# Optimization experiments

Measured on AMD Instinct MI355X. Metric: run time of the kernel, lower is better.

Reference implementation:

```python
import jax, jax.numpy as jnp
import numpy as np

USER_NUM = 100000
POI_NUM = 120
EMB = 64
HID1, HID2 = 256, 128
HEADS, ATT_H = 6, 8
SEQ = 5
CI_VOCAB = 50000
N_EDGES_U = 1600000


def _gcn_conv(x, edge_index, W, b, n):
    # PyG GCNConv: add self loops, symmetric D^-1/2 (A+I) D^-1/2 normalization
    x = x @ W
    loops = jnp.arange(n)
    src = jnp.concatenate([edge_index[0], loops])
    dst = jnp.concatenate([edge_index[1], loops])
    deg = jax.ops.segment_sum(jnp.ones_like(dst, x.dtype), dst, num_segments=n)
    dinv = jnp.where(deg > 0, jax.lax.rsqrt(deg), 0.0)
    norm = dinv[src] * dinv[dst]
    out = jax.ops.segment_sum(x[src] * norm[:, None], dst, num_segments=n)
    return out + b


def setup_inputs() -> dict:
    key = jax.random.key(0)
    ks = jax.random.split(key, 30)
    f = lambda k, shape, fan_in: (jax.random.normal(k, shape, jnp.float32) / np.sqrt(fan_in)).astype(jnp.float32)
    inp = {}
    inp['edge_user'] = jnp.stack([
        jax.random.randint(ks[0], (USER_NUM, SEQ), 0, USER_NUM),
        jax.random.randint(ks[1], (USER_NUM, SEQ), 0, CI_VOCAB)])
    inp['edge_poi'] = jax.random.randint(ks[2], (2, 4000), 0, POI_NUM)
    inp['u_v_edge'] = jax.random.randint(ks[3], (2, N_EDGES_U), 0, USER_NUM)
    inp['v_u_edge'] = jax.random.randint(ks[4], (2, 4000), 0, POI_NUM)
    inp['user_table'] = f(ks[5], (USER_NUM, EMB), EMB)
    inp['ci_table'] = f(ks[6], (CI_VOCAB, EMB), EMB)
    inp['ci_table2'] = f(ks[7], (CI_VOCAB, EMB), EMB)
    inp['gcn1_w'] = f(ks[8], (EMB, EMB), EMB)
    inp['gcn1_b'] = jnp.zeros((EMB,), jnp.float32)
    inp['gcn2_w'] = f(ks[9], (EMB, EMB), EMB)
    inp['gcn2_b'] = jnp.zeros((EMB,), jnp.float32)
    inp['at_w'] = f(ks[10], (HEADS, EMB, ATT_H), EMB)
    inp['at_b'] = jnp.zeros((HEADS, ATT_H), jnp.float32)
    inp['d2_w'] = f(ks[11], (1 + HEADS * ATT_H, 1), 1 + HEADS * ATT_H)  # Linear(49,1)
    inp['d2_b'] = jnp.zeros((1,), jnp.float32)
    inp['d1u_w'] = f(ks[12], (EMB, HID1), EMB)
    inp['d1u_b'] = jnp.zeros((HID1,), jnp.float32)
    inp['d2u_w'] = f(ks[13], (HID1, HID2), HID1)
    inp['d2u_b'] = jnp.zeros((HID2,), jnp.float32)
    inp['d3u_w'] = f(ks[14], (HID2, POI_NUM), HID2)
    inp['d3u_b'] = jnp.zeros((POI_NUM,), jnp.float32)
    inp['d1_w'] = f(ks[15], (EMB, POI_NUM), EMB)  # dense1_: Linear(n_emb, 120)
    inp['d1_b'] = jnp.zeros((POI_NUM,), jnp.float32)
    return inp


def reference(edge_user, edge_poi, u_v_edge, v_u_edge, user_table, ci_table, ci_table2,
              gcn1_w, gcn1_b, gcn2_w, gcn2_b, at_w, at_b, d2_w, d2_b,
              d1u_w, d1u_b, d2u_w, d2u_b, d3u_w, d3u_b, d1_w, d1_b):
    # user GCN stack (dropout treated as identity / eval mode)
    ue = _gcn_conv(user_table, u_v_edge, gcn1_w, gcn1_b, USER_NUM)
    ue = jax.nn.relu(ue)
    ue = _gcn_conv(ue, u_v_edge, gcn2_w, gcn2_b, USER_NUM)  # (U, EMB)

    ci_ids = edge_user[1]            # (U, SEQ) check-in ids
    ci = ci_table[ci_ids]            # (U, SEQ, EMB)
    ci2 = ci_table2[ci_ids]          # (U, SEQ, EMB)

    # batched multi-head tiny attention: softmax over the SEQ axis per user
    w = jnp.einsum('usd,hdk->uhsk', ci, at_w) + at_b[None, :, None, :]
    beta = jax.nn.softmax(jnp.tanh(w), axis=2)                       # (U, H, SEQ, ATT_H)
    beta = jnp.transpose(beta, (0, 2, 1, 3)).reshape(ci.shape[0], SEQ, HEADS * ATT_H)
    att = jnp.transpose(beta, (0, 2, 1))                              # (U, 48, SEQ)
    use_trans = att @ ci                                              # (U, 48, EMB)

    uef = jnp.concatenate([ue[:, None, :], use_trans], axis=1)       # (U, 49, EMB)
    uef = jnp.transpose(uef, (0, 2, 1)) @ d2_w + d2_b                # (U, EMB, 1)
    uef = uef[..., 0]                                                # (U, EMB)

    h = jax.nn.relu(uef @ d1u_w + d1u_b)
    h = jax.nn.relu(h @ d2u_w + d2u_b)
    score1 = h @ d3u_w + d3u_b                                       # (U, POI_NUM)

    score2 = jnp.sum(ci2 @ d1_w + d1_b, axis=1)                      # (U, POI_NUM)
    return score1 + score2
```

## Files before the change

### kernel.cpp

```cpp
#include <hip/hip_runtime.h>

#define U_NUM 100000
#define NE    1600000
#define SEQL  5

#define OFF_DEG      0UL
#define OFF_ROWSTART 800000UL
#define OFF_DINV     1200016UL
#define OFF_BSUM     1600016UL
#define OFF_CSR      1600528UL
#define OFF_XS       8000528UL
#define OFF_B        20800528UL
#define OFF_CI2B     46400528UL
#define OFF_CIB      52800528UL

#define NB    196
#define BSH   9
#define BCAP  12240
#define OFF_BINS  OFF_XS
#define OFF_GCUR  (OFF_BINS + (size_t)NB * BCAP * 8)

typedef __attribute__((ext_vector_type(8))) short bf16x8;
typedef __attribute__((ext_vector_type(4))) float f32x4;
typedef __attribute__((ext_vector_type(4))) unsigned u32x4;

__device__ __forceinline__ float rd_lane(float v, int l) {
    return __int_as_float(__builtin_amdgcn_readlane(__float_as_int(v), l));
}

__device__ __forceinline__ short f2bf(float f) {
    unsigned u = __float_as_uint(f);
    unsigned r = (u + 0x7fffu + ((u >> 16) & 1u)) >> 16;
    return (short)r;
}

__device__ __forceinline__ unsigned pk2(float a, float b) {
    return ((unsigned)(unsigned short)f2bf(a)) | (((unsigned)(unsigned short)f2bf(b)) << 16);
}

__device__ __forceinline__ float bflo(unsigned p) { return __uint_as_float(p << 16); }
__device__ __forceinline__ float bfhi(unsigned p) { return __uint_as_float(p & 0xffff0000u); }

__device__ __forceinline__ int swzo(int row, int bytecol, int rowstride) {
    return row * rowstride + (bytecol ^ ((row & 7) << 4));
}

__global__ __launch_bounds__(256) void k_count(const int* __restrict__ edge, int* __restrict__ deg) {
    int e = blockIdx.x * 256 + threadIdx.x;
    atomicAdd(&deg[edge[NE + e]], 1);
}

__global__ __launch_bounds__(256) void k_dinv(const int* __restrict__ deg, float* __restrict__ dinv) {
    int i = blockIdx.x * 256 + threadIdx.x;
    if (i < U_NUM) dinv[i] = rsqrtf((float)(deg[i] + 1));
}

__global__ __launch_bounds__(256) void k_cvt2(const float* __restrict__ src, unsigned* __restrict__ dst) {
    int i = blockIdx.x * 256 + threadIdx.x;
    float2 v = *(const float2*)(src + (size_t)i * 2);
    dst[i] = pk2(v.x, v.y);
}

__global__ __launch_bounds__(1024) void k_scanA(const int* __restrict__ deg, int* __restrict__ bsum) {
    __shared__ int sm[1024];
    int i = blockIdx.x * 1024 + threadIdx.x;
    sm[threadIdx.x] = (i < U_NUM) ? deg[i] : 0;
    __syncthreads();
    for (int off = 512; off > 0; off >>= 1) {
        if (threadIdx.x < off) sm[threadIdx.x] += sm[threadIdx.x + off];
        __syncthreads();
    }
    if (threadIdx.x == 0) bsum[blockIdx.x] = sm[0];
}

__global__ void k_scanB(int* bsum, int nb) {
    if (threadIdx.x == 0) {
        int acc = 0;
        for (int b = 0; b < nb; ++b) { int v = bsum[b]; bsum[b] = acc; acc += v; }
    }
}

__global__ __launch_bounds__(1024) void k_scanC(const int* __restrict__ deg, const int* __restrict__ bsum,
                                                int* __restrict__ row_start) {
    __shared__ int sm[1024];
    int t = threadIdx.x;
    int i = blockIdx.x * 1024 + t;
    int v = (i < U_NUM) ? deg[i] : 0;
    sm[t] = v;
    __syncthreads();
    for (int off = 1; off < 1024; off <<= 1) {
        int x = (t >= off) ? sm[t - off] : 0;
        __syncthreads();
        sm[t] += x;
        __syncthreads();
    }
    int incl = sm[t];
    int base = bsum[blockIdx.x];
    if (i < U_NUM) row_start[i] = base + incl - v;
    if (i == U_NUM - 1) row_start[U_NUM] = base + incl;
}

__global__ __launch_bounds__(256) void k_binA(const int* __restrict__ edge,
                                              unsigned* __restrict__ gcur,
                                              uint2* __restrict__ bins) {
    __shared__ int hist[256];
    __shared__ int startx[256];
    __shared__ int cur[256];
    __shared__ int gbase[256];
    __shared__ uint2 stage[4096];
    int t = threadIdx.x;
    int base = blockIdx.x * 4096;
    hist[t] = 0; cur[t] = 0;
    __syncthreads();
    int src[16], dst[16];
#pragma unroll
    for (int j = 0; j < 16; ++j) {
        int e = base + j * 256 + t;
        src[j] = 0; dst[j] = -1;
        if (e < NE) {
            src[j] = edge[e];
            dst[j] = edge[NE + e];
            atomicAdd(&hist[dst[j] >> BSH], 1);
        }
    }
    __syncthreads();
    startx[t] = hist[t];
    __syncthreads();
    for (int off = 1; off < 256; off <<= 1) {
        int v = (t >= off) ? startx[t - off] : 0;
        __syncthreads();
        startx[t] += v;
        __syncthreads();
    }
    {
        int ex = startx[t] - hist[t];
        __syncthreads();
        startx[t] = ex;
    }
    if (t < NB) gbase[t] = (int)atomicAdd(&gcur[t], (unsigned)hist[t]);
    __syncthreads();
#pragma unroll
    for (int j = 0; j < 16; ++j) {
        if (dst[j] >= 0) {
            int b = dst[j] >> BSH;
            int p = startx[b] + atomicAdd(&cur[b], 1);
            stage[p] = make_uint2((unsigned)src[j], (unsigned)dst[j]);
        }
    }
    __syncthreads();
    int cnt = NE - base; if (cnt > 4096) cnt = 4096;
    for (int p = t; p < cnt; p += 256) {
        uint2 v = stage[p];
        int b = (int)(v.y >> BSH);
        bins[(size_t)b * BCAP + gbase[b] + (p - startx[b])] = v;
    }
}

__global__ __launch_bounds__(256) void k_fillB(const uint2* __restrict__ bins,
                                               const unsigned* __restrict__ gcur,
                                               const int* __restrict__ row_start,
                                               int* __restrict__ csr) {
    __shared__ int cur[512];
    int b = blockIdx.x, t = threadIdx.x;
    cur[t] = 0; cur[t + 256] = 0;
    __syncthreads();
    int cnt = (int)gcur[b];
    int d0 = b << BSH;
    for (int i = t; i < cnt; i += 256) {
        uint2 e = bins[(size_t)b * BCAP + i];
        int d = (int)e.y;
        int pos = row_start[d] + atomicAdd(&cur[d - d0], 1);
        csr[pos] = (int)e.x;
    }
}

__global__ __launch_bounds__(256) void k_gemm64_mfma(
        const float* __restrict__ x, const float* __restrict__ w,
        const float* __restrict__ dinv, unsigned* __restrict__ outb, int relu_in) {
    __shared__ __align__(16) short Xa[64 * 64];
    __shared__ float dv[64];
    int t = threadIdx.x;
    int lane = t & 63, wid = t >> 6;
    int l15 = lane & 15, lg = lane >> 4;
    bf16x8 wf[2];
#pragma unroll
    for (int ks = 0; ks < 2; ++ks) {
        int col = wid * 16 + l15;
        int kb = ks * 32 + lg * 8;
        bf16x8 f;
#pragma unroll
        for (int j = 0; j < 8; ++j) f[j] = f2bf(w[(kb + j) * 64 + col]);
        wf[ks] = f;
    }
    int u0 = blockIdx.x * 64;
    {
        int ur = t >> 2, d0 = (t & 3) * 16;
        int u = u0 + ur;
        float xv[16];
        if (u < U_NUM) {
            const float4* up = (const float4*)(x + (size_t)u * 64 + d0);
#pragma unroll
            for (int q = 0; q < 4; ++q) {
                float4 v = up[q];
                xv[q * 4 + 0] = v.x; xv[q * 4 + 1] = v.y; xv[q * 4 + 2] = v.z; xv[q * 4 + 3] = v.w;
            }
        } else {
#pragma unroll
            for (int q = 0; q < 16; ++q) xv[q] = 0.f;
        }
        if (relu_in) {
#pragma unroll
            for (int q = 0; q < 16; ++q) xv[q] = fmaxf(xv[q], 0.f);
        }
        bf16x8 p0, p1;
#pragma unroll
        for (int j = 0; j < 8; ++j) { p0[j] = f2bf(xv[j]); p1[j] = f2bf(xv[8 + j]); }
        *(bf16x8*)((char*)Xa + swzo(ur, d0 * 2, 128)) = p0;
        *(bf16x8*)((char*)Xa + swzo(ur, d0 * 2 + 16, 128)) = p1;
        if (t < 64) {
            int uu = u0 + t;
            dv[t] = dinv[(uu < U_NUM) ? uu : (U_NUM - 1)];
        }
    }
    __syncthreads();
#pragma unroll
    for (int mt = 0; mt < 4; ++mt) {
        bf16x8 a0 = *(bf16x8*)((char*)Xa + swzo(mt * 16 + l15, lg * 16, 128));
        bf16x8 a1 = *(bf16x8*)((char*)Xa + swzo(mt * 16 + l15, 64 + lg * 16, 128));
        f32x4 c = {0.f, 0.f, 0.f, 0.f};
        c = __builtin_amdgcn_mfma_f32_16x16x32_bf16(a0, wf[0], c, 0, 0, 0);
        c = __builtin_amdgcn_mfma_f32_16x16x32_bf16(a1, wf[1], c, 0, 0, 0);
        int col = wid * 16 + l15;
#pragma unroll
        for (int r = 0; r < 4; ++r) {
            int row = mt * 16 + lg * 4 + r;
            float v = c[r] * dv[row];
            float other = __shfl_xor(v, 1);
            int u = u0 + row;
            if (!(l15 & 1) && u < U_NUM)
                outb[(size_t)u * 32 + (col >> 1)] = pk2(v, other);
        }
    }
}

__global__ __launch_bounds__(256) void k_gather2(const unsigned* __restrict__ xs, const float* __restrict__ dinv,
                                                 const int* __restrict__ row_start, const int* __restrict__ csr,
                                                 const float* __restrict__ bias, float* __restrict__ outb) {
    int i = blockIdx.x * 4 + (threadIdx.x >> 6);
    int lane = threadIdx.x & 63, half = lane >> 5, sl = lane & 31;
    int s0 = row_start[i], s1 = row_start[i + 1];
    float di = dinv[i];
    float accx = 0.f, accy = 0.f;
    if (!half) {
        unsigned pk = xs[(size_t)i * 32 + sl];
        accx = bflo(pk); accy = bfhi(pk);
    }
    int e = s0 + half;
    for (; e + 14 < s1; e += 16) {
        int id0 = csr[e], id1 = csr[e + 2], id2 = csr[e + 4], id3 = csr[e + 6];
        int id4 = csr[e + 8], id5 = csr[e + 10], id6 = csr[e + 12], id7 = csr[e + 14];
        unsigned p0 = xs[(size_t)id0 * 32 + sl];
        unsigned p1 = xs[(size_t)id1 * 32 + sl];
        unsigned p2 = xs[(size_t)id2 * 32 + sl];
        unsigned p3 = xs[(size_t)id3 * 32 + sl];
        unsigned p4 = xs[(size_t)id4 * 32 + sl];
        unsigned p5 = xs[(size_t)id5 * 32 + sl];
        unsigned p6 = xs[(size_t)id6 * 32 + sl];
        unsigned p7 = xs[(size_t)id7 * 32 + sl];
        accx += ((bflo(p0) + bflo(p1)) + (bflo(p2) + bflo(p3))) +
                ((bflo(p4) + bflo(p5)) + (bflo(p6) + bflo(p7)));
        accy += ((bfhi(p0) + bfhi(p1)) + (bfhi(p2) + bfhi(p3))) +
                ((bfhi(p4) + bfhi(p5)) + (bfhi(p6) + bfhi(p7)));
    }
    for (; e < s1; e += 2) {
        unsigned pa = xs[(size_t)csr[e] * 32 + sl];
        accx += bflo(pa);
        accy += bfhi(pa);
    }
    accx += __shfl_xor(accx, 32);
    accy += __shfl_xor(accy, 32);
    if (!half) {
        float2 bb = *(const float2*)(bias + sl * 2);
        float2 o;
        o.x = fmaf(accx, di, bb.x);
        o.y = fmaf(accy, di, bb.y);
        *(float2*)(outb + (size_t)i * 64 + sl * 2) = o;
    }
}

#define AUB 32

__global__ __launch_bounds__(256) void k_attn_mfma(
        const int* __restrict__ edge_user, const unsigned* __restrict__ cib,
        const unsigned* __restrict__ ci2b,
        const float* __restrict__ at_w, const float* __restrict__ at_b,
        const float* __restrict__ d2_w, const float* __restrict__ d2_b,
        const float* ue, unsigned* uefc) {
    __shared__ __align__(16) short CI[256 * 64];
    int t = threadIdx.x;
    int lane = t & 63, wid = t >> 6;
    int l15 = lane & 15, lg = lane >> 4;
    int half = lane >> 5, sl = lane & 31;

    bf16x8 bw[3][2];
#pragma unroll
    for (int nt = 0; nt < 3; ++nt) {
        int j48 = nt * 16 + l15;
        int h = j48 >> 3, kk = j48 & 7;
#pragma unroll
        for (int ks = 0; ks < 2; ++ks) {
            int kb = ks * 32 + lg * 8;
            bf16x8 f;
#pragma unroll
            for (int j = 0; j < 8; ++j) f[j] = f2bf(at_w[h * 512 + (kb + j) * 8 + kk]);
            bw[nt][ks] = f;
        }
    }
    float atbv[3], dcoef[3];
#pragma unroll
    for (int nt = 0; nt < 3; ++nt) {
        atbv[nt] = at_b[nt * 16 + l15];
        dcoef[nt] = d2_w[1 + nt * 16 + l15];
    }
    float d2w0 = d2_w[0], d2b0 = d2_b[0];

    int u0 = blockIdx.x * AUB;
    float accx[8], accy[8];
#pragma unroll
    for (int j = 0; j < 8; ++j) { accx[j] = 0.f; accy[j] = 0.f; }
#pragma unroll
    for (int j = 0; j < 8; ++j) {
#pragma unroll
        for (int q = 0; q < 4; ++q) {
            int s = q * 2 + half;
            int row = wid * 64 + j * 8 + s;
            unsigned pk = 0;
            if (s < 5) {
                int id = edge_user[U_NUM * SEQL + (u0 + wid * 8 + j) * SEQL + s];
                pk = cib[(size_t)id * 32 + sl];
                unsigned pc = ci2b[(size_t)id * 32 + sl];
                accx[j] += bflo(pc);
                accy[j] += bfhi(pc);
            }
            *(unsigned*)((char*)CI + swzo(row, sl * 4, 128)) = pk;
        }
    }
    __syncthreads();

    float evenm = (lg & 1) ? 0.f : 1.f;
    for (int mt = 0; mt < 4; ++mt) {
        int tbase = (wid * 4 + mt) * 16;
        bf16x8 a0 = *(bf16x8*)((char*)CI + swzo(tbase + l15, lg * 16, 128));
        bf16x8 a1 = *(bf16x8*)((char*)CI + swzo(tbase + l15, 64 + lg * 16, 128));
        float g0 = 0.f, g1 = 0.f, g2 = 0.f, g3 = 0.f;
#pragma unroll
        for (int nt = 0; nt < 3; ++nt) {
            f32x4 c = {0.f, 0.f, 0.f, 0.f};
            c = __builtin_amdgcn_mfma_f32_16x16x32_bf16(a0, bw[nt][0], c, 0, 0, 0);
            c = __builtin_amdgcn_mfma_f32_16x16x32_bf16(a1, bw[nt][1], c, 0, 0, 0);
            float w0 = c[0] + atbv[nt], w1 = c[1] + atbv[nt],
                  w2 = c[2] + atbv[nt], w3 = c[3] + atbv[nt];
            float e0 = __expf(1.f - __fdividef(2.f, __expf(2.f * w0) + 1.f));
            float e1 = __expf(1.f - __fdividef(2.f, __expf(2.f * w1) + 1.f));
            float e2 = __expf(1.f - __fdividef(2.f, __expf(2.f * w2) + 1.f));
            float e3 = __expf(1.f - __fdividef(2.f, __expf(2.f * w3) + 1.f));
            float partial = e0 + evenm * (e1 + e2 + e3);
            float esum = partial + __shfl_xor(partial, 16);
            float sc = __fdividef(dcoef[nt], esum);
            g0 = fmaf(e0, sc, g0);
            g1 = fmaf(e1, sc, g1);
            g2 = fmaf(e2, sc, g2);
            g3 = fmaf(e3, sc, g3);
        }
#pragma unroll
        for (int d = 1; d < 16; d <<= 1) {
            g0 += __shfl_xor(g0, d);
            g1 += __shfl_xor(g1, d);
            g2 += __shfl_xor(g2, d);
            g3 += __shfl_xor(g3, d);
        }
        float gA0 = rd_lane(g0, 0), gA1 = rd_lane(g1, 0), gA2 = rd_lane(g2, 0),
              gA3 = rd_lane(g3, 0), gA4 = rd_lane(g0, 16);
        float gB0 = rd_lane(g0, 32), gB1 = rd_lane(g1, 32), gB2 = rd_lane(g2, 32),
              gB3 = rd_lane(g3, 32), gB4 = rd_lane(g0, 48);
        float gs0 = half ? gB0 : gA0;
        float gs1 = half ? gB1 : gA1;
        float gs2 = half ? gB2 : gA2;
        float gs3 = half ? gB3 : gA3;
        float gs4 = half ? gB4 : gA4;
        int urow = tbase + half * 8;
        int u = u0 + (tbase >> 3) + half;
        float2 uev = *(const float2*)(ue + (size_t)u * 64 + sl * 2);
        float rx = fmaf(d2w0, uev.x, d2b0);
        float ry = fmaf(d2w0, uev.y, d2b0);
        unsigned c0 = *(unsigned*)((char*)CI + swzo(urow + 0, sl * 4, 128));
        unsigned c1 = *(unsigned*)((char*)CI + swzo(urow + 1, sl * 4, 128));
        unsigned c2 = *(unsigned*)((char*)CI + swzo(urow + 2, sl * 4, 128));
        unsigned c3 = *(unsigned*)((char*)CI + swzo(urow + 3, sl * 4, 128));
        unsigned c4 = *(unsigned*)((char*)CI + swzo(urow + 4, sl * 4, 128));
        rx = fmaf(gs0, bflo(c0), rx); ry = fmaf(gs0, bfhi(c0), ry);
        rx = fmaf(gs1, bflo(c1), rx); ry = fmaf(gs1, bfhi(c1), ry);
        rx = fmaf(gs2, bflo(c2), rx); ry = fmaf(gs2, bfhi(c2), ry);
        rx = fmaf(gs3, bflo(c3), rx); ry = fmaf(gs3, bfhi(c3), ry);
        rx = fmaf(gs4, bflo(c4), rx); ry = fmaf(gs4, bfhi(c4), ry);
        uefc[(size_t)u * 64 + sl] = pk2(rx, ry);
    }
#pragma unroll
    for (int j = 0; j < 8; ++j) {
        float ax = accx[j] + __shfl_xor(accx[j], 32);
        float ay = accy[j] + __shfl_xor(accy[j], 32);
        if (!half) {
            int u = u0 + wid * 8 + j;
            uefc[(size_t)u * 64 + 32 + sl] = pk2(ax, ay);
        }
    }
}

#define N_TILES 1563

__global__ __launch_bounds__(512, 4) void k_mlp_mfma(
        const unsigned* __restrict__ uefc,
        const float* __restrict__ w1, const float* __restrict__ b1,
        const float* __restrict__ w2, const float* __restrict__ b2,
        const float* __restrict__ w3, const float* __restrict__ b3,
        const float* __restrict__ dw, const float* __restrict__ db,
        float* __restrict__ out) {
    __shared__ __align__(16) short Xa[64 * 64];
    __shared__ __align__(16) short Ca[64 * 64];
    __shared__ __align__(16) short h1a[64 * 256];
    __shared__ __align__(16) short h2c[64 * 128];
    int t = threadIdx.x;
    int lane = t & 63, w = t >> 6;
    int l15 = lane & 15, lg = lane >> 4;

    bf16x8 wf1[4];
#pragma unroll
    for (int nt = 0; nt < 2; ++nt)
#pragma unroll
        for (int ks = 0; ks < 2; ++ks) {
            int col = w * 32 + nt * 16 + l15;
            int kb = ks * 32 + lg * 8;
            bf16x8 f;
#pragma unroll
            for (int j = 0; j < 8; ++j) f[j] = f2bf(w1[(kb + j) * 256 + col]);
            wf1[nt * 2 + ks] = f;
        }
    bf16x8 wf2[8];
#pragma unroll
    for (int ks = 0; ks < 8; ++ks) {
        int col = w * 16 + l15;
        int kb = ks * 32 + lg * 8;
        bf16x8 f;
#pragma unroll
        for (int j = 0; j < 8; ++j) f[j] = f2bf(w2[(kb + j) * 128 + col]);
        wf2[ks] = f;
    }
    bf16x8 wf3[6];
#pragma unroll
    for (int ks = 0; ks < 6; ++ks) {
        int col = w * 16 + l15;
        int kb = ks * 32 + lg * 8;
        bf16x8 f;
#pragma unroll
        for (int j = 0; j < 8; ++j) {
            int k = kb + j;
            float v = 0.f;
            if (col < 120) v = (k < 128) ? w3[k * 120 + col] : dw[(k - 128) * 120 + col];
            f[j] = f2bf(v);
        }
        wf3[ks] = f;
    }
    float bias1[2], bias2, bias3;
#pragma unroll
    for (int nt = 0; nt < 2; ++nt) bias1[nt] = b1[w * 32 + nt * 16 + l15];
    {
        int col = w * 16 + l15;
        bias2 = b2[col];
        bias3 = (col < 120) ? (b3[col] + 5.f * db[col]) : 0.f;
    }

    int ur = t >> 3, q = t & 7;
    for (int tile = blockIdx.x; tile < N_TILES; tile += gridDim.x) {
        int u0 = tile * 64;
        {
            size_t u = (size_t)u0 + ur;
            u32x4 A0 = {0, 0, 0, 0}, A1 = A0;
            if (u < U_NUM) {
                const u32x4* up = (const u32x4*)(uefc + u * 64 + q * 8);
                A0 = __builtin_nontemporal_load(up);
                A1 = __builtin_nontemporal_load(up + 1);
            }
            char* base = (q < 4) ? ((char*)Xa) : ((char*)Ca);
            int bc = (q & 3) * 32;
            *(u32x4*)(base + swzo(ur, bc, 128)) = A0;
            *(u32x4*)(base + swzo(ur, bc + 16, 128)) = A1;
        }
        __syncthreads();
#pragma unroll
        for (int mt = 0; mt < 4; ++mt) {
            bf16x8 a0 = *(bf16x8*)((char*)Xa + swzo(mt * 16 + l15, lg * 16, 128));
            bf16x8 a1 = *(bf16x8*)((char*)Xa + swzo(mt * 16 + l15, 64 + lg * 16, 128));
#pragma unroll
            for (int nt = 0; nt < 2; ++nt) {
                f32x4 c = {0.f, 0.f, 0.f, 0.f};
                c = __builtin_amdgcn_mfma_f32_16x16x32_bf16(a0, wf1[nt * 2 + 0], c, 0, 0, 0);
                c = __builtin_amdgcn_mfma_f32_16x16x32_bf16(a1, wf1[nt * 2 + 1], c, 0, 0, 0);
                int col = w * 32 + nt * 16 + l15;
                float bb = bias1[nt];
#pragma unroll
                for (int r = 0; r < 4; ++r) {
                    int row = mt * 16 + lg * 4 + r;
                    *(short*)((char*)h1a + swzo(row, col * 2, 512)) = f2bf(fmaxf(c[r] + bb, 0.f));
                }
            }
        }
        __syncthreads();
#pragma unroll
        for (int mt = 0; mt < 4; ++mt) {
            bf16x8 af[8];
#pragma unroll
            for (int ks = 0; ks < 8; ++ks)
                af[ks] = *(bf16x8*)((char*)h1a + swzo(mt * 16 + l15, ks * 64 + lg * 16, 512));
            f32x4 c = {0.f, 0.f, 0.f, 0.f};
#pragma unroll
            for (int ks = 0; ks < 8; ++ks)
                c = __builtin_amdgcn_mfma_f32_16x16x32_bf16(af[ks], wf2[ks], c, 0, 0, 0);
            int col = w * 16 + l15;
#pragma unroll
            for (int r = 0; r < 4; ++r) {
                int row = mt * 16 + lg * 4 + r;
                *(short*)((char*)h2c + swzo(row, col * 2, 256)) = f2bf(fmaxf(c[r] + bias2, 0.f));
            }
        }
        __syncthreads();
        float* Obuf = (float*)h1a;
#pragma unroll
        for (int mt = 0; mt < 4; ++mt) {
            bf16x8 af[6];
#pragma unroll
            for (int ks = 0; ks < 4; ++ks)
                af[ks] = *(bf16x8*)((char*)h2c + swzo(mt * 16 + l15, ks * 64 + lg * 16, 256));
#pragma unroll
            for (int ks = 4; ks < 6; ++ks)
                af[ks] = *(bf16x8*)((char*)Ca + swzo(mt * 16 + l15, (ks - 4) * 64 + lg * 16, 128));
            f32x4 c = {0.f, 0.f, 0.f, 0.f};
#pragma unroll
            for (int ks = 0; ks < 6; ++ks)
                c = __builtin_amdgcn_mfma_f32_16x16x32_bf16(af[ks], wf3[ks], c, 0, 0, 0);
            int col = w * 16 + l15;
            if (col < 120) {
#pragma unroll
                for (int r = 0; r < 4; ++r)
                    Obuf[(mt * 16 + lg * 4 + r) * 124 + col] = c[r] + bias3;
            }
        }
        __syncthreads();
        {
            int nrow = (U_NUM - u0 < 64) ? (U_NUM - u0) : 64;
            int nfl4 = nrow * 30;
            for (int i = t; i < nfl4; i += 512) {
                int row = i / 30, ch = i - row * 30;
                f32x4 v = *(const f32x4*)(Obuf + row * 124 + ch * 4);
                __builtin_nontemporal_store(v, (f32x4*)(out + (size_t)(u0 + row) * 120 + ch * 4));
            }
        }
        __syncthreads();
    }
}

extern "C" void kernel_launch(void* const* d_in, const int* in_sizes, int n_in,
                              void* d_out, int out_size, void* d_ws, size_t ws_size,
                              hipStream_t stream) {
    const int* edge_user   = (const int*)d_in[0];
    const int* u_v_edge    = (const int*)d_in[2];
    const float* user_table = (const float*)d_in[4];
    const float* ci_table   = (const float*)d_in[5];
    const float* ci_table2  = (const float*)d_in[6];
    const float* gcn1_w = (const float*)d_in[7];
    const float* gcn1_b = (const float*)d_in[8];
    const float* gcn2_w = (const float*)d_in[9];
    const float* gcn2_b = (const float*)d_in[10];
    const float* at_w = (const float*)d_in[11];
    const float* at_b = (const float*)d_in[12];
    const float* d2_w = (const float*)d_in[13];
    const float* d2_b = (const float*)d_in[14];
    const float* d1u_w = (const float*)d_in[15];
    const float* d1u_b = (const float*)d_in[16];
    const float* d2u_w = (const float*)d_in[17];
    const float* d2u_b = (const float*)d_in[18];
    const float* d3u_w = (const float*)d_in[19];
    const float* d3u_b = (const float*)d_in[20];
    const float* d1_w = (const float*)d_in[21];
    const float* d1_b = (const float*)d_in[22];
    float* out = (float*)d_out;
    char* ws = (char*)d_ws;

    int* deg       = (int*)(ws + OFF_DEG);
    int* row_start = (int*)(ws + OFF_ROWSTART);
    float* dinv    = (float*)(ws + OFF_DINV);
    int* bsum      = (int*)(ws + OFF_BSUM);
    int* csr       = (int*)(ws + OFF_CSR);
    unsigned* XS   = (unsigned*)(ws + OFF_XS);
    float* B       = (float*)(ws + OFF_B);
    unsigned* CI2B = (unsigned*)(ws + OFF_CI2B);
    unsigned* CIB  = (unsigned*)(ws + OFF_CIB);
    uint2* bins    = (uint2*)(ws + OFF_BINS);
    unsigned* gcur = (unsigned*)(ws + OFF_GCUR);

    (void)hipMemsetAsync(ws, 0, 400000, stream);
    (void)hipMemsetAsync(ws + OFF_GCUR, 0, NB * 4, stream);
    k_count<<<6250, 256, 0, stream>>>(u_v_edge, deg);
    k_cvt2<<<6250, 256, 0, stream>>>(ci_table, CIB);
    k_cvt2<<<6250, 256, 0, stream>>>(ci_table2, CI2B);
    k_dinv<<<391, 256, 0, stream>>>(deg, dinv);
    k_scanA<<<98, 1024, 0, stream>>>(deg, bsum);
    k_scanB<<<1, 64, 0, stream>>>(bsum, 98);
    k_scanC<<<98, 1024, 0, stream>>>(deg, bsum, row_start);
    k_binA<<<391, 256, 0, stream>>>(u_v_edge, gcur, bins);
    k_fillB<<<NB, 256, 0, stream>>>(bins, gcur, row_start, csr);

    k_gemm64_mfma<<<1563, 256, 0, stream>>>(user_table, gcn1_w, dinv, XS, 0);
    k_gather2<<<25000, 256, 0, stream>>>(XS, dinv, row_start, csr, gcn1_b, B);
    k_gemm64_mfma<<<1563, 256, 0, stream>>>(B, gcn2_w, dinv, XS, 1);
    k_gather2<<<25000, 256, 0, stream>>>(XS, dinv, row_start, csr, gcn2_b, B);

    k_attn_mfma<<<3125, 256, 0, stream>>>(edge_user, CIB, CI2B, at_w, at_b, d2_w, d2_b,
                                          B, (unsigned*)B);
    k_mlp_mfma<<<512, 512, 0, stream>>>((const unsigned*)B,
                                        d1u_w, d1u_b, d2u_w, d2u_b, d3u_w, d3u_b, d1_w, d1_b, out);
}
```

Measured before the change: 468.9 us.

## Restructure MLP kernel to 32-row tiles with 16 waves and split-K reductions

The final MLP kernel now processes 32-user tiles with 1024-thread blocks. Layers 2 and 3 are split along K across two wave groups, and the partial sums are combined through a shared float buffer. Each wave holds fewer weight fragments, which cuts register pressure and raises parallelism per tile. The cost is extra barriers and LDS round-trips per tile. The tail check is dropped, which is safe only because 100000 divides evenly by 32.

```diff
diff --git a/kernel.cpp b/kernel.cpp
--- a/kernel.cpp
+++ b/kernel.cpp
@@ -22,7 +22,7 @@
 
 typedef __attribute__((ext_vector_type(8))) short bf16x8;
 typedef __attribute__((ext_vector_type(4))) float f32x4;
-typedef __attribute__((ext_vector_type(4))) unsigned u32x4;
+typedef __attribute__((ext_vector_type(2))) unsigned u32x2;
 
 __device__ __forceinline__ float rd_lane(float v, int l) {
     return __int_as_float(__builtin_amdgcn_readlane(__float_as_int(v), l));
@@ -416,153 +416,150 @@
     }
 }
 
-#define N_TILES 1563
-
-__global__ __launch_bounds__(512, 4) void k_mlp_mfma(
+#define N_TILES2 3125
+
+__global__ __launch_bounds__(1024, 2) void k_mlp_mfma(
         const unsigned* __restrict__ uefc,
         const float* __restrict__ w1, const float* __restrict__ b1,
         const float* __restrict__ w2, const float* __restrict__ b2,
         const float* __restrict__ w3, const float* __restrict__ b3,
         const float* __restrict__ dw, const float* __restrict__ db,
         float* __restrict__ out) {
-    __shared__ __align__(16) short Xa[64 * 64];
-    __shared__ __align__(16) short Ca[64 * 64];
-    __shared__ __align__(16) short h1a[64 * 256];
-    __shared__ __align__(16) short h2c[64 * 128];
+    __shared__ __align__(16) short Xa[32 * 64];
+    __shared__ __align__(16) short Ca[32 * 64];
+    __shared__ __align__(16) short h1a[32 * 256];
+    __shared__ __align__(16) short h2c[32 * 128];
+    __shared__ __align__(16) float Pf[32 * 128];
     int t = threadIdx.x;
     int lane = t & 63, w = t >> 6;
     int l15 = lane & 15, lg = lane >> 4;
-
-    bf16x8 wf1[4];
-#pragma unroll
-    for (int nt = 0; nt < 2; ++nt)
-#pragma unroll
-        for (int ks = 0; ks < 2; ++ks) {
-            int col = w * 32 + nt * 16 + l15;
-            int kb = ks * 32 + lg * 8;
-            bf16x8 f;
-#pragma unroll
-            for (int j = 0; j < 8; ++j) f[j] = f2bf(w1[(kb + j) * 256 + col]);
-            wf1[nt * 2 + ks] = f;
-        }
-    bf16x8 wf2[8];
-#pragma unroll
-    for (int ks = 0; ks < 8; ++ks) {
-        int col = w * 16 + l15;
+    int nt = w & 7, kh = w >> 3;
+    int col1 = w * 16 + l15;
+    int col2 = nt * 16 + l15;
+
+    bf16x8 wf1[2];
+#pragma unroll
+    for (int ks = 0; ks < 2; ++ks) {
         int kb = ks * 32 + lg * 8;
         bf16x8 f;
 #pragma unroll
-        for (int j = 0; j < 8; ++j) f[j] = f2bf(w2[(kb + j) * 128 + col]);
+        for (int j = 0; j < 8; ++j) f[j] = f2bf(w1[(kb + j) * 256 + col1]);
+        wf1[ks] = f;
+    }
+    bf16x8 wf2[4];
+#pragma unroll
+    for (int ks = 0; ks < 4; ++ks) {
+        int kb = kh * 128 + ks * 32 + lg * 8;
+        bf16x8 f;
+#pragma unroll
+        for (int j = 0; j < 8; ++j) f[j] = f2bf(w2[(kb + j) * 128 + col2]);
         wf2[ks] = f;
     }
-    bf16x8 wf3[6];
-#pragma unroll
-    for (int ks = 0; ks < 6; ++ks) {
-        int col = w * 16 + l15;
-        int kb = ks * 32 + lg * 8;
+    bf16x8 wf3[3];
+#pragma unroll
+    for (int ks = 0; ks < 3; ++ks) {
         bf16x8 f;
 #pragma unroll
         for (int j = 0; j < 8; ++j) {
-            int k = kb + j;
+            int k = kh * 96 + ks * 32 + lg * 8 + j;
             float v = 0.f;
-            if (col < 120) v = (k < 128) ? w3[k * 120 + col] : dw[(k - 128) * 120 + col];
+            if (col2 < 120) v = (k < 128) ? w3[k * 120 + col2] : dw[(k - 128) * 120 + col2];
             f[j] = f2bf(v);
         }
         wf3[ks] = f;
     }
-    float bias1[2], bias2, bias3;
-#pragma unroll
-    for (int nt = 0; nt < 2; ++nt) bias1[nt] = b1[w * 32 + nt * 16 + l15];
-    {
-        int col = w * 16 + l15;
-        bias2 = b2[col];
-        bias3 = (col < 120) ? (b3[col] + 5.f * db[col]) : 0.f;
-    }
-
-    int ur = t >> 3, q = t & 7;
-    for (int tile = blockIdx.x; tile < N_TILES; tile += gridDim.x) {
-        int u0 = tile * 64;
+    float bias1 = b1[col1];
+    float bias2 = b2[col2];
+    float bias3 = (col2 < 120) ? (b3[col2] + 5.f * db[col2]) : 0.f;
+
+    int ur = t >> 5, q = t & 31;
+    for (int tile = blockIdx.x; tile < N_TILES2; tile += gridDim.x) {
+        int u0 = tile * 32;
         {
-            size_t u = (size_t)u0 + ur;
-            u32x4 A0 = {0, 0, 0, 0}, A1 = A0;
-            if (u < U_NUM) {
-                const u32x4* up = (const u32x4*)(uefc + u * 64 + q * 8);
-                A0 = __builtin_nontemporal_load(up);
-                A1 = __builtin_nontemporal_load(up + 1);
-            }
-            char* base = (q < 4) ? ((char*)Xa) : ((char*)Ca);
-            int bc = (q & 3) * 32;
-            *(u32x4*)(base + swzo(ur, bc, 128)) = A0;
-            *(u32x4*)(base + swzo(ur, bc + 16, 128)) = A1;
-        }
-        __syncthreads();
-#pragma unroll
-        for (int mt = 0; mt < 4; ++mt) {
+            const u32x2* up = (const u32x2*)(uefc + (size_t)(u0 + ur) * 64 + q * 2);
+            u32x2 A = __builtin_nontemporal_load(up);
+            char* base = (q < 16) ? ((char*)Xa) : ((char*)Ca);
+            *(u32x2*)(base + swzo(ur, (q & 15) * 8, 128)) = A;
+        }
+        __syncthreads();
+#pragma unroll
+        for (int mt = 0; mt < 2; ++mt) {
             bf16x8 a0 = *(bf16x8*)((char*)Xa + swzo(mt * 16 + l15, lg * 16, 128));
             bf16x8 a1 = *(bf16x8*)((char*)Xa + swzo(mt * 16 + l15, 64 + lg * 16, 128));
-#pragma unroll
-            for (int nt = 0; nt < 2; ++nt) {
-                f32x4 c = {0.f, 0.f, 0.f, 0.f};
-                c = __builtin_amdgcn_mfma_f32_16x16x32_bf16(a0, wf1[nt * 2 + 0], c, 0, 0, 0);
-                c = __builtin_amdgcn_mfma_f32_16x16x32_bf16(a1, wf1[nt * 2 + 1], c, 0, 0, 0);
-                int col = w * 32 + nt * 16 + l15;
-                float bb = bias1[nt];
-#pragma unroll
-                for (int r = 0; r < 4; ++r) {
-                    int row = mt * 16 + lg * 4 + r;
-                    *(short*)((char*)h1a + swzo(row, col * 2, 512)) = f2bf(fmaxf(c[r] + bb, 0.f));
-                }
-            }
-        }
-        __syncthreads();
-#pragma unroll
-        for (int mt = 0; mt < 4; ++mt) {
-            bf16x8 af[8];
-#pragma unroll
-            for (int ks = 0; ks < 8; ++ks)
-                af[ks] = *(bf16x8*)((char*)h1a + swzo(mt * 16 + l15, ks * 64 + lg * 16, 512));
             f32x4 c = {0.f, 0.f, 0.f, 0.f};
-#pragma unroll
-            for (int ks = 0; ks < 8; ++ks)
-                c = __builtin_amdgcn_mfma_f32_16x16x32_bf16(af[ks], wf2[ks], c, 0, 0, 0);
-            int col = w * 16 + l15;
+            c = __builtin_amdgcn_mfma_f32_16x16x32_bf16(a0, wf1[0], c, 0, 0, 0);
+            c = __builtin_amdgcn_mfma_f32_16x16x32_bf16(a1, wf1[1], c, 0, 0, 0);
 #pragma unroll
             for (int r = 0; r < 4; ++r) {
                 int row = mt * 16 + lg * 4 + r;
-                *(short*)((char*)h2c + swzo(row, col * 2, 256)) = f2bf(fmaxf(c[r] + bias2, 0.f));
-            }
-        }
-        __syncthreads();
-        float* Obuf = (float*)h1a;
-#pragma unroll
-        for (int mt = 0; mt < 4; ++mt) {
-            bf16x8 af[6];
-#pragma unroll
-            for (int ks = 0; ks < 4; ++ks)
-                af[ks] = *(bf16x8*)((char*)h2c + swzo(mt * 16 + l15, ks * 64 + lg * 16, 256));
-#pragma unroll
-            for (int ks = 4; ks < 6; ++ks)
-                af[ks] = *(bf16x8*)((char*)Ca + swzo(mt * 16 + l15, (ks - 4) * 64 + lg * 16, 128));
-            f32x4 c = {0.f, 0.f, 0.f, 0.f};
-#pragma unroll
-            for (int ks = 0; ks < 6; ++ks)
-                c = __builtin_amdgcn_mfma_f32_16x16x32_bf16(af[ks], wf3[ks], c, 0, 0, 0);
-            int col = w * 16 + l15;
-            if (col < 120) {
-#pragma unroll
-                for (int r = 0; r < 4; ++r)
-                    Obuf[(mt * 16 + lg * 4 + r) * 124 + col] = c[r] + bias3;
-            }
-        }
-        __syncthreads();
-        {
-            int nrow = (U_NUM - u0 < 64) ? (U_NUM - u0) : 64;
-            int nfl4 = nrow * 30;
-            for (int i = t; i < nfl4; i += 512) {
-                int row = i / 30, ch = i - row * 30;
-                f32x4 v = *(const f32x4*)(Obuf + row * 124 + ch * 4);
-                __builtin_nontemporal_store(v, (f32x4*)(out + (size_t)(u0 + row) * 120 + ch * 4));
-            }
+                *(short*)((char*)h1a + swzo(row, col1 * 2, 512)) = f2bf(fmaxf(c[r] + bias1, 0.f));
+            }
+        }
+        __syncthreads();
+        f32x4 c20 = {0.f, 0.f, 0.f, 0.f}, c21 = c20;
+#pragma unroll
+        for (int ks = 0; ks < 4; ++ks) {
+            int bc = kh * 256 + ks * 64 + lg * 16;
+            bf16x8 a0 = *(bf16x8*)((char*)h1a + swzo(l15, bc, 512));
+            bf16x8 a1 = *(bf16x8*)((char*)h1a + swzo(16 + l15, bc, 512));
+            c20 = __builtin_amdgcn_mfma_f32_16x16x32_bf16(a0, wf2[ks], c20, 0, 0, 0);
+            c21 = __builtin_amdgcn_mfma_f32_16x16x32_bf16(a1, wf2[ks], c21, 0, 0, 0);
+        }
+        if (kh == 0) {
+#pragma unroll
+            for (int r = 0; r < 4; ++r) {
+                Pf[(lg * 4 + r) * 128 + col2] = c20[r];
+                Pf[(16 + lg * 4 + r) * 128 + col2] = c21[r];
+            }
+        }
+        __syncthreads();
+        if (kh == 1) {
+#pragma unroll
+            for (int r = 0; r < 4; ++r) {
+                float s0 = c20[r] + Pf[(lg * 4 + r) * 128 + col2];
+                float s1 = c21[r] + Pf[(16 + lg * 4 + r) * 128 + col2];
+                *(short*)((char*)h2c + swzo(lg * 4 + r, col2 * 2, 256)) = f2bf(fmaxf(s0 + bias2, 0.f));
+                *(short*)((char*)h2c + swzo(16 + lg * 4 + r, col2 * 2, 256)) = f2bf(fmaxf(s1 + bias2, 0.f));
+            }
+        }
+        __syncthreads();
+        f32x4 c30 = {0.f, 0.f, 0.f, 0.f}, c31 = c30;
+#pragma unroll
+        for (int ks = 0; ks < 3; ++ks) {
+            int k0 = kh * 96 + ks * 32;
+            bf16x8 a0, a1;
+            if (k0 < 128) {
+                a0 = *(bf16x8*)((char*)h2c + swzo(l15, k0 * 2 + lg * 16, 256));
+                a1 = *(bf16x8*)((char*)h2c + swzo(16 + l15, k0 * 2 + lg * 16, 256));
+            } else {
+                a0 = *(bf16x8*)((char*)Ca + swzo(l15, (k0 - 128) * 2 + lg * 16, 128));
+                a1 = *(bf16x8*)((char*)Ca + swzo(16 + l15, (k0 - 128) * 2 + lg * 16, 128));
+            }
+            c30 = __builtin_amdgcn_mfma_f32_16x16x32_bf16(a0, wf3[ks], c30, 0, 0, 0);
+            c31 = __builtin_amdgcn_mfma_f32_16x16x32_bf16(a1, wf3[ks], c31, 0, 0, 0);
+        }
+        if (kh == 0) {
+#pragma unroll
+            for (int r = 0; r < 4; ++r) {
+                Pf[(lg * 4 + r) * 128 + col2] = c30[r];
+                Pf[(16 + lg * 4 + r) * 128 + col2] = c31[r];
+            }
+        }
+        __syncthreads();
+        if (kh == 1) {
+#pragma unroll
+            for (int r = 0; r < 4; ++r) {
+                int rowa = (lg * 4 + r) * 128 + col2;
+                int rowb = (16 + lg * 4 + r) * 128 + col2;
+                Pf[rowa] = c30[r] + Pf[rowa] + bias3;
+                Pf[rowb] = c31[r] + Pf[rowb] + bias3;
+            }
+        }
+        __syncthreads();
+        if (t < 960) {
+            int row = t / 30, ch = t - row * 30;
+            f32x4 v = *(const f32x4*)(Pf + row * 128 + ch * 4);
+            __builtin_nontemporal_store(v, (f32x4*)(out + (size_t)(u0 + row) * 120 + ch * 4));
         }
         __syncthreads();
     }
@@ -626,6 +623,6 @@
 
     k_attn_mfma<<<3125, 256, 0, stream>>>(edge_user, CIB, CI2B, at_w, at_b, d2_w, d2_b,
                                           B, (unsigned*)B);
-    k_mlp_mfma<<<512, 512, 0, stream>>>((const unsigned*)B,
-                                        d1u_w, d1u_b, d2u_w, d2u_b, d3u_w, d3u_b, d1_w, d1_b, out);
-}
+    k_mlp_mfma<<<512, 1024, 0, stream>>>((const unsigned*)B,
+                                         d1u_w, d1u_b, d2u_w, d2u_b, d3u_w, d3u_b, d1_w, d1_b, out);
+}
```

Measured after the change: 424.8 us. 1.1x faster.
